# Kernel optimization log

Measured on AMD Instinct MI355X. Metric: run time of the kernel, lower is better.

The kernel has to match this reference:

```python
import jax, jax.numpy as jnp
import numpy as np

EPS = 1e-6
MAX_ACOSH_ARG = 1e6
MAX_DIST = 50.0
TINY = 1e-15
B, T, D = 2, 512, 512
H, N = 8, 32
A = N + 1
TAU = 1.0


def mink(x, y):
    # Lorentzian inner product over last (ambient) dim
    return -x[..., 0] * y[..., 0] + jnp.sum(x[..., 1:] * y[..., 1:], axis=-1)


def project_to_hyperboloid(x):
    xx = mink(x, x)
    scale = jnp.sqrt(jnp.maximum(jnp.abs(xx), TINY))[..., None]
    x = x / scale
    return jnp.concatenate([jnp.abs(x[..., :1]), x[..., 1:]], axis=-1)


def exp_map(p, v):
    vn = jnp.sqrt(jnp.maximum(mink(v, v), TINY))[..., None]
    y = jnp.cosh(vn) * p + (jnp.sinh(vn) / jnp.maximum(vn, TINY)) * v
    return project_to_hyperboloid(y)


def log_map(p, y):
    alpha = jnp.clip(-mink(p, y), 1.0 + EPS, MAX_ACOSH_ARG)
    dist = jnp.arccosh(alpha)[..., None]
    u = y + alpha[..., None] * p
    un = jnp.sqrt(jnp.maximum(mink(u, u), TINY))[..., None]
    return dist / jnp.maximum(un, TINY) * u


def _lift(x, W, b):
    # Linear lift -> (B,H,T,N), append time-like 0, expmap at origin
    u = (jnp.einsum('btd,dk->btk', x, W) + b).reshape(B, T, H, N).transpose(0, 2, 1, 3)
    v = jnp.concatenate([jnp.zeros(u.shape[:-1] + (1,), u.dtype), u], axis=-1)  # (B,H,T,A)
    o = jnp.zeros((A,), u.dtype).at[0].set(1.0)
    return exp_map(jnp.broadcast_to(o, v.shape), v)


def setup_inputs() -> dict:
    key = jax.random.key(0)
    ks = jax.random.split(key, 5)
    x = jax.random.normal(ks[0], (B, T, D), jnp.float32)
    Wq = jax.random.normal(ks[1], (D, H * N), jnp.float32) * 0.02
    Wk = jax.random.normal(ks[2], (D, H * N), jnp.float32) * 0.02
    Wv = jax.random.normal(ks[3], (D, H * N), jnp.float32) * 0.02
    Wo = jax.random.normal(ks[4], (H * A, D), jnp.float32) * 0.02
    return {'x': x, 'Wq': Wq, 'bq': jnp.zeros((H * N,), jnp.float32),
            'Wk': Wk, 'bk': jnp.zeros((H * N,), jnp.float32),
            'Wv': Wv, 'bv': jnp.zeros((H * N,), jnp.float32),
            'Wo': Wo, 'bo': jnp.zeros((D,), jnp.float32)}


def reference(x, Wq, bq, Wk, bk, Wv, bv, Wo, bo):
    Q = _lift(x, Wq, bq)  # (B,H,T,A) on hyperboloid
    K = _lift(x, Wk, bk)
    V = _lift(x, Wv, bv)

    # pairwise hyperbolic distances: alpha = -<q,k>_L, d = acosh(alpha)
    alpha = jnp.clip(-mink(Q[:, :, :, None, :], K[:, :, None, :, :]), 1.0 + EPS, MAX_ACOSH_ARG)
    d = jnp.minimum(jnp.arccosh(alpha), MAX_DIST)  # (B,H,T,T)
    scores = -TAU * d * d
    attn = jax.nn.softmax(scores.astype(jnp.float32), axis=-1).astype(V.dtype)

    # one Karcher step around Q
    Y = Q
    logv = log_map(Y[:, :, :, None, :], V[:, :, None, :, :])  # (B,H,T,T,A)
    step = jnp.einsum('bhqk,bhqka->bhqa', attn, logv)
    step_norm = jnp.sqrt(jnp.maximum(mink(step, step), TINY))[..., None]
    step = step * (jnp.minimum(step_norm, 20.0) / (step_norm + 1e-9))
    Y = exp_map(Y, step)  # (B,H,T,A)

    # log-map at origin anchor, project back to d_model
    o = jnp.zeros((A,), Y.dtype).at[0].set(1.0)
    Yt = Y.transpose(0, 2, 1, 3)  # (B,T,H,A)
    p0 = jnp.broadcast_to(o, Yt.shape)
    Z_tan = log_map(p0, Yt).reshape(B, T, H * A)
    Z = jnp.einsum('btk,kd->btd', Z_tan, Wo) + bo
    return Z
```

## Files before the change

### kernel.cpp

```cpp
#include <hip/hip_runtime.h>
#include <math.h>

#define EPSF 1e-6f
#define MAX_ACOSH_ARGF 1e6f
#define MAX_DISTF 50.0f
#define TINYF 1e-15f

typedef float f4v __attribute__((ext_vector_type(4)));
typedef float f2v __attribute__((ext_vector_type(2)));

constexpr int QPSZ = 16 * 512 * 36;
constexpr int KTSZ = 16 * 9 * 512 * 4;
constexpr int ZTSZ = 1024 * 264;

__device__ __forceinline__ float facosh(float a) {
    return __logf(a + sqrtf((a - 1.0f) * (a + 1.0f)));
}

__global__ __launch_bounds__(64) void qkv_kernel(
    const float* __restrict__ x,
    const float* __restrict__ Wq, const float* __restrict__ bq,
    const float* __restrict__ Wk, const float* __restrict__ bk,
    const float* __restrict__ Wv, const float* __restrict__ bv,
    float* __restrict__ Qp, float* __restrict__ KT, float* __restrict__ VT)
{
    const int lane = threadIdx.x;
    const int gw   = blockIdx.x;
    const int ct   = gw % 6;
    const int mt   = gw / 6;
    const int m0   = mt * 4;
    const int tsel = ct >> 1;
    const int n0   = (ct & 1) * 128;
    const float* W    = (tsel == 0) ? Wq : (tsel == 1) ? Wk : Wv;
    const float* bias = (tsel == 0) ? bq : (tsel == 1) ? bk : bv;
    const int c0 = n0 + lane * 2;
    const float* xb = x + m0 * 512;

    float acc[4][2];
    {
        const float b0 = bias[c0], b1 = bias[c0 + 1];
        #pragma unroll
        for (int r = 0; r < 4; ++r) { acc[r][0] = b0; acc[r][1] = b1; }
    }

    f4v aA[4][2], aB[4][2];
    f2v bA[8], bB[8];

#define LDA_Q(BUF, KB)                                            \
    _Pragma("unroll") for (int r = 0; r < 4; ++r) {               \
        BUF[r][0] = *(const f4v*)(xb + r * 512 + (KB));           \
        BUF[r][1] = *(const f4v*)(xb + r * 512 + (KB) + 4);       \
    }
#define LDB_Q(BUF, KB)                                            \
    _Pragma("unroll") for (int j = 0; j < 8; ++j)                 \
        BUF[j] = *(const f2v*)(W + ((KB) + j) * 256 + c0);
#define STEP_Q(AB, BB)                                            \
    _Pragma("unroll") for (int j = 0; j < 8; ++j) {               \
        _Pragma("unroll") for (int r = 0; r < 4; ++r) {           \
            const float av = AB[r][j >> 2][j & 3];                \
            acc[r][0] = fmaf(av, BB[j][0], acc[r][0]);            \
            acc[r][1] = fmaf(av, BB[j][1], acc[r][1]);            \
        }                                                         \
    }

    LDA_Q(aA, 0) LDB_Q(bA, 0)
    for (int kb = 0; kb < 512; kb += 16) {
        LDA_Q(aB, kb + 8) LDB_Q(bB, kb + 8)
        STEP_Q(aA, bA)
        if (kb + 16 < 512) { LDA_Q(aA, kb + 16) LDB_Q(bA, kb + 16) }
        STEP_Q(aB, bB)
    }

    const int h   = c0 >> 5;
    const int cin = c0 & 31;
    #pragma unroll
    for (int r = 0; r < 4; ++r) {
        const float e0 = acc[r][0], e1 = acc[r][1];
        float n2 = fmaf(e0, e0, e1 * e1);
        #pragma unroll
        for (int msk = 1; msk < 16; msk <<= 1) n2 += __shfl_xor(n2, msk, 64);
        n2 = fmaxf(n2, TINYF);
        const float vn = sqrtf(n2);
        const float ch = coshf(vn);
        const float sh = sinhf(vn) / fmaxf(vn, TINYF);
        const float xx = fmaf(sh * sh, n2, -ch * ch);
        const float scale = sqrtf(fmaxf(fabsf(xx), TINYF));
        const float fs = sh / scale;
        const int bt = m0 + r, b = bt >> 9, t = bt & 511;
        const int bh = b * 8 + h;
        if (tsel == 0) {
            float* qp = Qp + (bh * 512 + t) * 36;
            qp[1 + cin] = fs * e0;
            qp[2 + cin] = fs * e1;
            if (cin == 0)  qp[0] = fabsf(ch / scale);
            if (cin == 30) { qp[33] = 0.0f; qp[34] = 0.0f; qp[35] = 0.0f; }
        } else {
            float* P = ((tsel == 1) ? KT : VT) + bh * 18432;
            const int aa = 1 + cin, ab = 2 + cin;
            P[(aa >> 2) * 2048 + t * 4 + (aa & 3)] = fs * e0;
            P[(ab >> 2) * 2048 + t * 4 + (ab & 3)] = fs * e1;
            if (cin == 0)  P[t * 4] = fabsf(ch / scale);
            if (cin == 30) {
                P[8 * 2048 + t * 4 + 1] = 0.0f;
                P[8 * 2048 + t * 4 + 2] = 0.0f;
                P[8 * 2048 + t * 4 + 3] = 0.0f;
            }
        }
    }
}

__global__ __launch_bounds__(256) void attn_kernel(
    const float* __restrict__ Qp, const float* __restrict__ KT,
    const float* __restrict__ VT, float* __restrict__ ZT)
{
    const int tid  = threadIdx.x;
    const int blk  = blockIdx.x;
    const int bh   = blk >> 5;
    const int q0   = (blk & 31) * 16;
    const int wid  = tid >> 6;
    const int lane = tid & 63;
    const int g    = lane >> 4;
    const int t    = lane & 15;
    const int qi   = q0 + wid * 4 + g;

    float qn[36];
    {
        const float* qp = Qp + (bh * 512 + qi) * 36;
        #pragma unroll
        for (int j = 0; j < 9; ++j) {
            const f4v v = *(const f4v*)(qp + 4 * j);
            #pragma unroll
            for (int i = 0; i < 4; ++i) {
                const int a = 4 * j + i;
                qn[a] = (a == 0) ? v[i] : -v[i];
            }
        }
    }

    const f4v* K4 = (const f4v*)KT + bh * 4608;
    const f4v* V4 = (const f4v*)VT + bh * 4608;

    float m = -3.0e38f, l = 0.0f, s = 0.0f;
    float ac[33];
    #pragma unroll
    for (int a = 0; a < 33; ++a) ac[a] = 0.0f;

    for (int st = 0; st < 32; ++st) {
        const int k = t + 16 * st;
        f4v kr[9], vr[9];
        #pragma unroll
        for (int j = 0; j < 9; ++j) kr[j] = K4[j * 512 + k];
        #pragma unroll
        for (int j = 0; j < 9; ++j) vr[j] = V4[j * 512 + k];

        float p0 = 0.f, p1 = 0.f, p2 = 0.f, p3 = 0.f;
        #pragma unroll
        for (int j = 0; j < 9; ++j) {
            p0 = fmaf(qn[4 * j],     kr[j][0], p0);
            p1 = fmaf(qn[4 * j + 1], kr[j][1], p1);
            p2 = fmaf(qn[4 * j + 2], kr[j][2], p2);
            p3 = fmaf(qn[4 * j + 3], kr[j][3], p3);
        }
        const float a1 = (p0 + p1) + (p2 + p3);

        float r0 = 0.f, r1 = 0.f, r2 = 0.f, r3 = 0.f;
        #pragma unroll
        for (int j = 0; j < 9; ++j) {
            r0 = fmaf(qn[4 * j],     vr[j][0], r0);
            r1 = fmaf(qn[4 * j + 1], vr[j][1], r1);
            r2 = fmaf(qn[4 * j + 2], vr[j][2], r2);
            r3 = fmaf(qn[4 * j + 3], vr[j][3], r3);
        }
        const float a2 = (r0 + r1) + (r2 + r3);

        const float a1c = fminf(fmaxf(a1, 1.0f + EPSF), MAX_ACOSH_ARGF);
        const float d1  = fminf(facosh(a1c), MAX_DISTF);
        const float sN  = -d1 * d1;
        const float a2c = fminf(fmaxf(a2, 1.0f + EPSF), MAX_ACOSH_ARGF);
        const float d2  = facosh(a2c);

        if (sN > m) {
            const float cr = __expf(m - sN);
            l *= cr; s *= cr;
            #pragma unroll
            for (int a = 0; a < 33; ++a) ac[a] *= cr;
            m = sN;
        }
        const float e = __expf(sN - m);
        l += e;
        const float w = e * d2;
        s = fmaf(w, a2c, s);
        #pragma unroll
        for (int a = 0; a < 33; ++a) ac[a] = fmaf(w, vr[a >> 2][a & 3], ac[a]);
    }

    float M = m;
    #pragma unroll
    for (int msk = 1; msk < 16; msk <<= 1) M = fmaxf(M, __shfl_xor(M, msk, 64));
    const float cl = __expf(m - M);
    float lw = l * cl, sw = s * cl;
    #pragma unroll
    for (int msk = 1; msk < 16; msk <<= 1) {
        lw += __shfl_xor(lw, msk, 64);
        sw += __shfl_xor(sw, msk, 64);
    }
    #pragma unroll
    for (int a = 0; a < 33; ++a) {
        float v = ac[a] * cl;
        #pragma unroll
        for (int msk = 1; msk < 16; msk <<= 1) v += __shfl_xor(v, msk, 64);
        ac[a] = v;
    }

    const float un_c  = sqrtf(TINYF);
    const float inv_un = (1.0f / lw) / un_c;
    ac[0] = fmaf(sw, qn[0], ac[0]) * inv_un;
    #pragma unroll
    for (int a = 1; a < 33; ++a) ac[a] = fmaf(-sw, qn[a], ac[a]) * inv_un;

    float mk = -ac[0] * ac[0];
    #pragma unroll
    for (int a = 1; a < 33; ++a) mk = fmaf(ac[a], ac[a], mk);
    const float snorm = sqrtf(fmaxf(mk, TINYF));
    const float fac   = fminf(snorm, 20.0f) / (snorm + 1e-9f);
    #pragma unroll
    for (int a = 0; a < 33; ++a) ac[a] *= fac;

    float mk2 = -ac[0] * ac[0];
    #pragma unroll
    for (int a = 1; a < 33; ++a) mk2 = fmaf(ac[a], ac[a], mk2);
    const float vn  = sqrtf(fmaxf(mk2, TINYF));
    const float ch  = coshf(vn);
    const float shr = sinhf(vn) / fmaxf(vn, TINYF);
    ac[0] = fmaf(ch, qn[0], shr * ac[0]);
    #pragma unroll
    for (int a = 1; a < 33; ++a) ac[a] = fmaf(-ch, qn[a], shr * ac[a]);

    float xx = -ac[0] * ac[0];
    #pragma unroll
    for (int a = 1; a < 33; ++a) xx = fmaf(ac[a], ac[a], xx);
    const float scale = sqrtf(fmaxf(fabsf(xx), TINYF));

    const float Y0  = fabsf(ac[0] / scale);
    const float al3 = fminf(fmaxf(Y0, 1.0f + EPSF), MAX_ACOSH_ARGF);
    const float d3  = acoshf(al3);
    const float f3  = d3 / un_c;

    if (t == 0) {
        const int b = bh >> 3, h = bh & 7;
        float* zp = ZT + (b * 512 + qi) * 264 + h * 33;
        zp[0] = f3 * (Y0 + al3);
        const float fsc = f3 / scale;
        #pragma unroll
        for (int a = 1; a < 33; ++a) zp[a] = fsc * ac[a];
    }
}

__global__ __launch_bounds__(64) void out_kernel(
    const float* __restrict__ ZT, const float* __restrict__ Wo,
    const float* __restrict__ bo, float* __restrict__ out)
{
    const int lane = threadIdx.x;
    const int gw   = blockIdx.x;
    const int mt   = gw >> 2;
    const int m0   = mt * 4;
    const int n0   = (gw & 3) * 128;
    const int c0   = n0 + lane * 2;
    const float* zb = ZT + m0 * 264;

    float acc[4][2];
    {
        const float b0 = bo[c0], b1 = bo[c0 + 1];
        #pragma unroll
        for (int r = 0; r < 4; ++r) { acc[r][0] = b0; acc[r][1] = b1; }
    }

    f4v aA[4][2], aB[4][2];
    f2v bA[8], bB[8];

#define LDA_O(BUF, KB)                                            \
    _Pragma("unroll") for (int r = 0; r < 4; ++r) {               \
        BUF[r][0] = *(const f4v*)(zb + r * 264 + (KB));           \
        BUF[r][1] = *(const f4v*)(zb + r * 264 + (KB) + 4);       \
    }
#define LDB_O(BUF, KB)                                            \
    _Pragma("unroll") for (int j = 0; j < 8; ++j)                 \
        BUF[j] = *(const f2v*)(Wo + ((KB) + j) * 512 + c0);
#define STEP_O(AB, BB)                                            \
    _Pragma("unroll") for (int j = 0; j < 8; ++j) {               \
        _Pragma("unroll") for (int r = 0; r < 4; ++r) {           \
            const float av = AB[r][j >> 2][j & 3];                \
            acc[r][0] = fmaf(av, BB[j][0], acc[r][0]);            \
            acc[r][1] = fmaf(av, BB[j][1], acc[r][1]);            \
        }                                                         \
    }

    LDA_O(aA, 0) LDB_O(bA, 0)
    for (int kb = 0; kb < 256; kb += 16) {
        LDA_O(aB, kb + 8) LDB_O(bB, kb + 8)
        STEP_O(aA, bA)
        LDA_O(aA, kb + 16) LDB_O(bA, kb + 16)
        STEP_O(aB, bB)
    }
    STEP_O(aA, bA)

    #pragma unroll
    for (int r = 0; r < 4; ++r)
        *(f2v*)(out + (m0 + r) * 512 + c0) = f2v{acc[r][0], acc[r][1]};
}

extern "C" void kernel_launch(void* const* d_in, const int* in_sizes, int n_in,
                              void* d_out, int out_size, void* d_ws, size_t ws_size,
                              hipStream_t stream) {
    const float* x  = (const float*)d_in[0];
    const float* Wq = (const float*)d_in[1];
    const float* bq = (const float*)d_in[2];
    const float* Wk = (const float*)d_in[3];
    const float* bk = (const float*)d_in[4];
    const float* Wv = (const float*)d_in[5];
    const float* bv = (const float*)d_in[6];
    const float* Wo = (const float*)d_in[7];
    const float* bo = (const float*)d_in[8];
    float* out = (float*)d_out;
    float* ws  = (float*)d_ws;

    float* Qp  = ws;
    float* KT  = ws + QPSZ;
    float* VT  = ws + QPSZ + KTSZ;
    float* ZTp = ws + QPSZ + 2 * KTSZ;

    qkv_kernel<<<1536, 64, 0, stream>>>(x, Wq, bq, Wk, bk, Wv, bv, Qp, KT, VT);
    attn_kernel<<<512, 256, 0, stream>>>(Qp, KT, VT, ZTp);
    out_kernel<<<1024, 64, 0, stream>>>(ZTp, Wo, bo, out);
}
```

Baseline: 171.7 us.

## Rewrite attention with LDS-staged K/V chunks, two queries per wave, no online max

The attention kernel now stages K and V chunks of 64 keys in double-buffered shared memory. Each wave handles two queries across all 64 lanes, one key per lane, and the final reductions use DPP adds. The running-max softmax rescaling is dropped on the grounds that scores are at most zero, and the s accumulator is recomputed from the reduced sums as a dot with q. Q, K and V share one row-major layout. The QKV and output GEMMs move to a four-stage register prefetch ring. Dropping the max subtraction risks underflow when all scores are very negative, and the larger blocks with two accumulator sets raise register pressure.

```diff
diff --git a/kernel.cpp b/kernel.cpp
--- a/kernel.cpp
+++ b/kernel.cpp
@@ -9,12 +9,26 @@
 typedef float f4v __attribute__((ext_vector_type(4)));
 typedef float f2v __attribute__((ext_vector_type(2)));
 
-constexpr int QPSZ = 16 * 512 * 36;
-constexpr int KTSZ = 16 * 9 * 512 * 4;
-constexpr int ZTSZ = 1024 * 264;
+constexpr int TENS = 16 * 512 * 36;
 
 __device__ __forceinline__ float facosh(float a) {
     return __logf(a + sqrtf((a - 1.0f) * (a + 1.0f)));
+}
+__device__ __forceinline__ float bcast(float x) {
+    return __int_as_float(__builtin_amdgcn_readfirstlane(__float_as_int(x)));
+}
+template<int C> __device__ __forceinline__ float dpp_add(float x) {
+    int t = __builtin_amdgcn_update_dpp(0, __float_as_int(x), C, 0xf, 0xf, false);
+    return x + __int_as_float(t);
+}
+__device__ __forceinline__ float redsum64(float x) {
+    x = dpp_add<0x111>(x);
+    x = dpp_add<0x112>(x);
+    x = dpp_add<0x114>(x);
+    x = dpp_add<0x118>(x);
+    x = dpp_add<0x142>(x);
+    x = dpp_add<0x143>(x);
+    return x;
 }
 
 __global__ __launch_bounds__(64) void qkv_kernel(
@@ -22,7 +36,7 @@
     const float* __restrict__ Wq, const float* __restrict__ bq,
     const float* __restrict__ Wk, const float* __restrict__ bk,
     const float* __restrict__ Wv, const float* __restrict__ bv,
-    float* __restrict__ Qp, float* __restrict__ KT, float* __restrict__ VT)
+    float* __restrict__ Q, float* __restrict__ K, float* __restrict__ V)
 {
     const int lane = threadIdx.x;
     const int gw   = blockIdx.x;
@@ -33,6 +47,7 @@
     const int n0   = (ct & 1) * 128;
     const float* W    = (tsel == 0) ? Wq : (tsel == 1) ? Wk : Wv;
     const float* bias = (tsel == 0) ? bq : (tsel == 1) ? bk : bv;
+    float* OUT        = (tsel == 0) ? Q  : (tsel == 1) ? K  : V;
     const int c0 = n0 + lane * 2;
     const float* xb = x + m0 * 512;
 
@@ -43,33 +58,32 @@
         for (int r = 0; r < 4; ++r) { acc[r][0] = b0; acc[r][1] = b1; }
     }
 
-    f4v aA[4][2], aB[4][2];
-    f2v bA[8], bB[8];
-
-#define LDA_Q(BUF, KB)                                            \
-    _Pragma("unroll") for (int r = 0; r < 4; ++r) {               \
-        BUF[r][0] = *(const f4v*)(xb + r * 512 + (KB));           \
-        BUF[r][1] = *(const f4v*)(xb + r * 512 + (KB) + 4);       \
-    }
-#define LDB_Q(BUF, KB)                                            \
-    _Pragma("unroll") for (int j = 0; j < 8; ++j)                 \
-        BUF[j] = *(const f2v*)(W + ((KB) + j) * 256 + c0);
-#define STEP_Q(AB, BB)                                            \
-    _Pragma("unroll") for (int j = 0; j < 8; ++j) {               \
-        _Pragma("unroll") for (int r = 0; r < 4; ++r) {           \
-            const float av = AB[r][j >> 2][j & 3];                \
-            acc[r][0] = fmaf(av, BB[j][0], acc[r][0]);            \
-            acc[r][1] = fmaf(av, BB[j][1], acc[r][1]);            \
-        }                                                         \
-    }
-
-    LDA_Q(aA, 0) LDB_Q(bA, 0)
-    for (int kb = 0; kb < 512; kb += 16) {
-        LDA_Q(aB, kb + 8) LDB_Q(bB, kb + 8)
-        STEP_Q(aA, bA)
-        if (kb + 16 < 512) { LDA_Q(aA, kb + 16) LDB_Q(bA, kb + 16) }
-        STEP_Q(aB, bB)
-    }
+    f4v a[4][4][2];
+    f2v b[4][8];
+
+#define LDQ(B, KB)                                                      \
+    { _Pragma("unroll") for (int r = 0; r < 4; ++r) {                   \
+          a[B][r][0] = *(const f4v*)(xb + r * 512 + (KB));              \
+          a[B][r][1] = *(const f4v*)(xb + r * 512 + (KB) + 4); }        \
+      _Pragma("unroll") for (int j = 0; j < 8; ++j)                     \
+          b[B][j] = *(const f2v*)(W + ((KB) + j) * 256 + c0); }
+#define STQ(B)                                                          \
+    { _Pragma("unroll") for (int j = 0; j < 8; ++j) {                   \
+        _Pragma("unroll") for (int r = 0; r < 4; ++r) {                 \
+            const float av = a[B][r][j >> 2][j & 3];                    \
+            acc[r][0] = fmaf(av, b[B][j][0], acc[r][0]);                \
+            acc[r][1] = fmaf(av, b[B][j][1], acc[r][1]); } } }
+
+    LDQ(0, 0) LDQ(1, 8) LDQ(2, 16) LDQ(3, 24)
+    for (int kb = 0; kb < 480; kb += 32) {
+        STQ(0) LDQ(0, kb + 32)
+        STQ(1) LDQ(1, kb + 40)
+        STQ(2) LDQ(2, kb + 48)
+        STQ(3) LDQ(3, kb + 56)
+    }
+    STQ(0) STQ(1) STQ(2) STQ(3)
+#undef LDQ
+#undef STQ
 
     const int h   = c0 >> 5;
     const int cin = c0 & 31;
@@ -86,173 +100,196 @@
         const float xx = fmaf(sh * sh, n2, -ch * ch);
         const float scale = sqrtf(fmaxf(fabsf(xx), TINYF));
         const float fs = sh / scale;
-        const int bt = m0 + r, b = bt >> 9, t = bt & 511;
-        const int bh = b * 8 + h;
-        if (tsel == 0) {
-            float* qp = Qp + (bh * 512 + t) * 36;
-            qp[1 + cin] = fs * e0;
-            qp[2 + cin] = fs * e1;
-            if (cin == 0)  qp[0] = fabsf(ch / scale);
-            if (cin == 30) { qp[33] = 0.0f; qp[34] = 0.0f; qp[35] = 0.0f; }
-        } else {
-            float* P = ((tsel == 1) ? KT : VT) + bh * 18432;
-            const int aa = 1 + cin, ab = 2 + cin;
-            P[(aa >> 2) * 2048 + t * 4 + (aa & 3)] = fs * e0;
-            P[(ab >> 2) * 2048 + t * 4 + (ab & 3)] = fs * e1;
-            if (cin == 0)  P[t * 4] = fabsf(ch / scale);
-            if (cin == 30) {
-                P[8 * 2048 + t * 4 + 1] = 0.0f;
-                P[8 * 2048 + t * 4 + 2] = 0.0f;
-                P[8 * 2048 + t * 4 + 3] = 0.0f;
-            }
-        }
-    }
-}
-
-__global__ __launch_bounds__(256) void attn_kernel(
-    const float* __restrict__ Qp, const float* __restrict__ KT,
-    const float* __restrict__ VT, float* __restrict__ ZT)
+        const int bt = m0 + r, bb = bt >> 9, t = bt & 511;
+        float* rp = OUT + ((bb * 8 + h) * 512 + t) * 36;
+        rp[1 + cin] = fs * e0;
+        rp[2 + cin] = fs * e1;
+        if (cin == 0) {
+            rp[0] = fabsf(ch / scale);
+            rp[33] = 0.0f; rp[34] = 0.0f; rp[35] = 0.0f;
+        }
+    }
+}
+
+__global__ __launch_bounds__(512, 4) void attn_kernel(
+    const float* __restrict__ Qg, const float* __restrict__ Kg,
+    const float* __restrict__ Vg, float* __restrict__ ZT)
 {
-    const int tid  = threadIdx.x;
-    const int blk  = blockIdx.x;
-    const int bh   = blk >> 5;
-    const int q0   = (blk & 31) * 16;
-    const int wid  = tid >> 6;
+    __shared__ f4v skv[2][1152];
+    __shared__ f4v sQ4[144];
+
+    const int tid = threadIdx.x;
+    const int blk = blockIdx.x;
+    const int bh  = blk >> 5;
+    const int q0t = (blk & 31) * 16;
+    const int wid = __builtin_amdgcn_readfirstlane(tid >> 6);
     const int lane = tid & 63;
-    const int g    = lane >> 4;
-    const int t    = lane & 15;
-    const int qi   = q0 + wid * 4 + g;
-
-    float qn[36];
+
+    const f4v* K4 = (const f4v*)(Kg + bh * 512 * 36);
+    const f4v* V4 = (const f4v*)(Vg + bh * 512 * 36);
+
+    const f4v* s0 = K4 + tid;
+    const f4v* s1 = (tid < 64) ? (K4 + 512 + tid) : (V4 + (tid - 64));
+    const f4v* s2 = V4 + 448 + tid;
+    const int d0 = tid, d1 = tid + 512, d2 = tid + 1024;
+
+    skv[0][d0] = s0[0];
+    skv[0][d1] = s1[0];
+    if (tid < 128) skv[0][d2] = s2[0];
+    if (tid < 144) sQ4[tid] = ((const f4v*)(Qg + (bh * 512 + q0t) * 36))[tid];
+    __syncthreads();
+
+    float qn0[36], qn1[36];
     {
-        const float* qp = Qp + (bh * 512 + qi) * 36;
+        const float* qs = (const float*)sQ4;
+        #pragma unroll
+        for (int a2 = 0; a2 < 36; ++a2) {
+            const float v0 = qs[(2 * wid) * 36 + a2];
+            const float v1 = qs[(2 * wid + 1) * 36 + a2];
+            qn0[a2] = bcast(a2 ? -v0 : v0);
+            qn1[a2] = bcast(a2 ? -v1 : v1);
+        }
+    }
+
+    float l0 = 0.0f, l1 = 0.0f;
+    float ac0[33], ac1[33];
+    #pragma unroll
+    for (int a2 = 0; a2 < 33; ++a2) { ac0[a2] = 0.0f; ac1[a2] = 0.0f; }
+
+    for (int c = 0; c < 8; ++c) {
+        f4v p0, p1, p2;
+        const bool have = (c < 7);
+        if (have) {
+            p0 = s0[(c + 1) * 576];
+            p1 = s1[(c + 1) * 576];
+            if (tid < 128) p2 = s2[(c + 1) * 576];
+        }
+        const f4v* buf = skv[c & 1];
+        const f4v* kr = buf + lane * 9;
+        const f4v* vr = buf + 576 + lane * 9;
+
+        float x10 = 0.f, x11 = 0.f, x20 = 0.f, x21 = 0.f;
         #pragma unroll
         for (int j = 0; j < 9; ++j) {
-            const f4v v = *(const f4v*)(qp + 4 * j);
-            #pragma unroll
-            for (int i = 0; i < 4; ++i) {
-                const int a = 4 * j + i;
-                qn[a] = (a == 0) ? v[i] : -v[i];
-            }
-        }
-    }
-
-    const f4v* K4 = (const f4v*)KT + bh * 4608;
-    const f4v* V4 = (const f4v*)VT + bh * 4608;
-
-    float m = -3.0e38f, l = 0.0f, s = 0.0f;
-    float ac[33];
+            const f4v kv = kr[j];
+            x10 = fmaf(qn0[4 * j],     kv[0], x10);
+            x11 = fmaf(qn0[4 * j + 1], kv[1], x11);
+            x10 = fmaf(qn0[4 * j + 2], kv[2], x10);
+            x11 = fmaf(qn0[4 * j + 3], kv[3], x11);
+            x20 = fmaf(qn1[4 * j],     kv[0], x20);
+            x21 = fmaf(qn1[4 * j + 1], kv[1], x21);
+            x20 = fmaf(qn1[4 * j + 2], kv[2], x20);
+            x21 = fmaf(qn1[4 * j + 3], kv[3], x21);
+        }
+        const float a1q0 = x10 + x11, a1q1 = x20 + x21;
+
+        if (have) {
+            f4v* w = skv[(c + 1) & 1];
+            w[d0] = p0; w[d1] = p1;
+            if (tid < 128) w[d2] = p2;
+        }
+
+        f4v vf[9];
+        #pragma unroll
+        for (int j = 0; j < 9; ++j) vf[j] = vr[j];
+        float y10 = 0.f, y11 = 0.f, y20 = 0.f, y21 = 0.f;
+        #pragma unroll
+        for (int j = 0; j < 9; ++j) {
+            y10 = fmaf(qn0[4 * j],     vf[j][0], y10);
+            y11 = fmaf(qn0[4 * j + 1], vf[j][1], y11);
+            y10 = fmaf(qn0[4 * j + 2], vf[j][2], y10);
+            y11 = fmaf(qn0[4 * j + 3], vf[j][3], y11);
+            y20 = fmaf(qn1[4 * j],     vf[j][0], y20);
+            y21 = fmaf(qn1[4 * j + 1], vf[j][1], y21);
+            y20 = fmaf(qn1[4 * j + 2], vf[j][2], y20);
+            y21 = fmaf(qn1[4 * j + 3], vf[j][3], y21);
+        }
+        const float a2q0 = y10 + y11, a2q1 = y20 + y21;
+
+        {
+            const float a1c = fminf(fmaxf(a1q0, 1.0f + EPSF), MAX_ACOSH_ARGF);
+            const float dd  = fminf(facosh(a1c), MAX_DISTF);
+            const float e   = __expf(-dd * dd);
+            const float a2c = fminf(fmaxf(a2q0, 1.0f + EPSF), MAX_ACOSH_ARGF);
+            const float w0  = e * facosh(a2c);
+            l0 += e;
+            #pragma unroll
+            for (int a2 = 0; a2 < 33; ++a2)
+                ac0[a2] = fmaf(w0, vf[a2 >> 2][a2 & 3], ac0[a2]);
+        }
+        {
+            const float a1c = fminf(fmaxf(a1q1, 1.0f + EPSF), MAX_ACOSH_ARGF);
+            const float dd  = fminf(facosh(a1c), MAX_DISTF);
+            const float e   = __expf(-dd * dd);
+            const float a2c = fminf(fmaxf(a2q1, 1.0f + EPSF), MAX_ACOSH_ARGF);
+            const float w1  = e * facosh(a2c);
+            l1 += e;
+            #pragma unroll
+            for (int a2 = 0; a2 < 33; ++a2)
+                ac1[a2] = fmaf(w1, vf[a2 >> 2][a2 & 3], ac1[a2]);
+        }
+        __syncthreads();
+    }
+
+    const float lw0 = redsum64(l0);
+    const float lw1 = redsum64(l1);
     #pragma unroll
-    for (int a = 0; a < 33; ++a) ac[a] = 0.0f;
-
-    for (int st = 0; st < 32; ++st) {
-        const int k = t + 16 * st;
-        f4v kr[9], vr[9];
-        #pragma unroll
-        for (int j = 0; j < 9; ++j) kr[j] = K4[j * 512 + k];
-        #pragma unroll
-        for (int j = 0; j < 9; ++j) vr[j] = V4[j * 512 + k];
-
-        float p0 = 0.f, p1 = 0.f, p2 = 0.f, p3 = 0.f;
-        #pragma unroll
-        for (int j = 0; j < 9; ++j) {
-            p0 = fmaf(qn[4 * j],     kr[j][0], p0);
-            p1 = fmaf(qn[4 * j + 1], kr[j][1], p1);
-            p2 = fmaf(qn[4 * j + 2], kr[j][2], p2);
-            p3 = fmaf(qn[4 * j + 3], kr[j][3], p3);
-        }
-        const float a1 = (p0 + p1) + (p2 + p3);
-
-        float r0 = 0.f, r1 = 0.f, r2 = 0.f, r3 = 0.f;
-        #pragma unroll
-        for (int j = 0; j < 9; ++j) {
-            r0 = fmaf(qn[4 * j],     vr[j][0], r0);
-            r1 = fmaf(qn[4 * j + 1], vr[j][1], r1);
-            r2 = fmaf(qn[4 * j + 2], vr[j][2], r2);
-            r3 = fmaf(qn[4 * j + 3], vr[j][3], r3);
-        }
-        const float a2 = (r0 + r1) + (r2 + r3);
-
-        const float a1c = fminf(fmaxf(a1, 1.0f + EPSF), MAX_ACOSH_ARGF);
-        const float d1  = fminf(facosh(a1c), MAX_DISTF);
-        const float sN  = -d1 * d1;
-        const float a2c = fminf(fmaxf(a2, 1.0f + EPSF), MAX_ACOSH_ARGF);
-        const float d2  = facosh(a2c);
-
-        if (sN > m) {
-            const float cr = __expf(m - sN);
-            l *= cr; s *= cr;
-            #pragma unroll
-            for (int a = 0; a < 33; ++a) ac[a] *= cr;
-            m = sN;
-        }
-        const float e = __expf(sN - m);
-        l += e;
-        const float w = e * d2;
-        s = fmaf(w, a2c, s);
-        #pragma unroll
-        for (int a = 0; a < 33; ++a) ac[a] = fmaf(w, vr[a >> 2][a & 3], ac[a]);
-    }
-
-    float M = m;
-    #pragma unroll
-    for (int msk = 1; msk < 16; msk <<= 1) M = fmaxf(M, __shfl_xor(M, msk, 64));
-    const float cl = __expf(m - M);
-    float lw = l * cl, sw = s * cl;
-    #pragma unroll
-    for (int msk = 1; msk < 16; msk <<= 1) {
-        lw += __shfl_xor(lw, msk, 64);
-        sw += __shfl_xor(sw, msk, 64);
-    }
-    #pragma unroll
-    for (int a = 0; a < 33; ++a) {
-        float v = ac[a] * cl;
-        #pragma unroll
-        for (int msk = 1; msk < 16; msk <<= 1) v += __shfl_xor(v, msk, 64);
-        ac[a] = v;
-    }
-
-    const float un_c  = sqrtf(TINYF);
-    const float inv_un = (1.0f / lw) / un_c;
-    ac[0] = fmaf(sw, qn[0], ac[0]) * inv_un;
-    #pragma unroll
-    for (int a = 1; a < 33; ++a) ac[a] = fmaf(-sw, qn[a], ac[a]) * inv_un;
-
-    float mk = -ac[0] * ac[0];
-    #pragma unroll
-    for (int a = 1; a < 33; ++a) mk = fmaf(ac[a], ac[a], mk);
-    const float snorm = sqrtf(fmaxf(mk, TINYF));
-    const float fac   = fminf(snorm, 20.0f) / (snorm + 1e-9f);
-    #pragma unroll
-    for (int a = 0; a < 33; ++a) ac[a] *= fac;
-
-    float mk2 = -ac[0] * ac[0];
-    #pragma unroll
-    for (int a = 1; a < 33; ++a) mk2 = fmaf(ac[a], ac[a], mk2);
-    const float vn  = sqrtf(fmaxf(mk2, TINYF));
-    const float ch  = coshf(vn);
-    const float shr = sinhf(vn) / fmaxf(vn, TINYF);
-    ac[0] = fmaf(ch, qn[0], shr * ac[0]);
-    #pragma unroll
-    for (int a = 1; a < 33; ++a) ac[a] = fmaf(-ch, qn[a], shr * ac[a]);
-
-    float xx = -ac[0] * ac[0];
-    #pragma unroll
-    for (int a = 1; a < 33; ++a) xx = fmaf(ac[a], ac[a], xx);
-    const float scale = sqrtf(fmaxf(fabsf(xx), TINYF));
-
-    const float Y0  = fabsf(ac[0] / scale);
-    const float al3 = fminf(fmaxf(Y0, 1.0f + EPSF), MAX_ACOSH_ARGF);
-    const float d3  = acoshf(al3);
-    const float f3  = d3 / un_c;
-
-    if (t == 0) {
+    for (int a2 = 0; a2 < 33; ++a2) {
+        ac0[a2] = redsum64(ac0[a2]);
+        ac1[a2] = redsum64(ac1[a2]);
+    }
+
+    if (lane == 63) {
         const int b = bh >> 3, h = bh & 7;
-        float* zp = ZT + (b * 512 + qi) * 264 + h * 33;
-        zp[0] = f3 * (Y0 + al3);
-        const float fsc = f3 / scale;
-        #pragma unroll
-        for (int a = 1; a < 33; ++a) zp[a] = fsc * ac[a];
+        #pragma unroll
+        for (int q = 0; q < 2; ++q) {
+            float (&ac)[33] = q ? ac1 : ac0;
+            const float (&qn)[36] = q ? qn1 : qn0;
+            const float lw = q ? lw1 : lw0;
+            float sw = 0.0f;
+            #pragma unroll
+            for (int a2 = 0; a2 < 33; ++a2) sw = fmaf(qn[a2], ac[a2], sw);
+            const float un_c  = 3.1622776601683794e-8f;
+            const float inv_un = (1.0f / lw) / un_c;
+            ac[0] = fmaf(sw, qn[0], ac[0]) * inv_un;
+            #pragma unroll
+            for (int a2 = 1; a2 < 33; ++a2) ac[a2] = fmaf(-sw, qn[a2], ac[a2]) * inv_un;
+
+            float mk = -ac[0] * ac[0];
+            #pragma unroll
+            for (int a2 = 1; a2 < 33; ++a2) mk = fmaf(ac[a2], ac[a2], mk);
+            const float snorm = sqrtf(fmaxf(mk, TINYF));
+            const float fac   = fminf(snorm, 20.0f) / (snorm + 1e-9f);
+            #pragma unroll
+            for (int a2 = 0; a2 < 33; ++a2) ac[a2] *= fac;
+
+            float mk2 = -ac[0] * ac[0];
+            #pragma unroll
+            for (int a2 = 1; a2 < 33; ++a2) mk2 = fmaf(ac[a2], ac[a2], mk2);
+            const float vn  = sqrtf(fmaxf(mk2, TINYF));
+            const float ch  = coshf(vn);
+            const float shr = sinhf(vn) / fmaxf(vn, TINYF);
+            ac[0] = fmaf(ch, qn[0], shr * ac[0]);
+            #pragma unroll
+            for (int a2 = 1; a2 < 33; ++a2) ac[a2] = fmaf(-ch, qn[a2], shr * ac[a2]);
+
+            float xx = -ac[0] * ac[0];
+            #pragma unroll
+            for (int a2 = 1; a2 < 33; ++a2) xx = fmaf(ac[a2], ac[a2], xx);
+            const float scale = sqrtf(fmaxf(fabsf(xx), TINYF));
+
+            const float Y0  = fabsf(ac[0] / scale);
+            const float al3 = fminf(fmaxf(Y0, 1.0f + EPSF), MAX_ACOSH_ARGF);
+            const float d3  = acoshf(al3);
+            const float f3  = d3 / un_c;
+
+            const int qi = q0t + 2 * wid + q;
+            float* zp = ZT + (b * 512 + qi) * 264 + h * 33;
+            zp[0] = f3 * (Y0 + al3);
+            const float fsc = f3 / scale;
+            #pragma unroll
+            for (int a2 = 1; a2 < 33; ++a2) zp[a2] = fsc * ac[a2];
+        }
     }
 }
 
@@ -275,34 +312,34 @@
         for (int r = 0; r < 4; ++r) { acc[r][0] = b0; acc[r][1] = b1; }
     }
 
-    f4v aA[4][2], aB[4][2];
-    f2v bA[8], bB[8];
-
-#define LDA_O(BUF, KB)                                            \
-    _Pragma("unroll") for (int r = 0; r < 4; ++r) {               \
-        BUF[r][0] = *(const f4v*)(zb + r * 264 + (KB));           \
-        BUF[r][1] = *(const f4v*)(zb + r * 264 + (KB) + 4);       \
-    }
-#define LDB_O(BUF, KB)                                            \
-    _Pragma("unroll") for (int j = 0; j < 8; ++j)                 \
-        BUF[j] = *(const f2v*)(Wo + ((KB) + j) * 512 + c0);
-#define STEP_O(AB, BB)                                            \
-    _Pragma("unroll") for (int j = 0; j < 8; ++j) {               \
-        _Pragma("unroll") for (int r = 0; r < 4; ++r) {           \
-            const float av = AB[r][j >> 2][j & 3];                \
-            acc[r][0] = fmaf(av, BB[j][0], acc[r][0]);            \
-            acc[r][1] = fmaf(av, BB[j][1], acc[r][1]);            \
-        }                                                         \
-    }
-
-    LDA_O(aA, 0) LDB_O(bA, 0)
-    for (int kb = 0; kb < 256; kb += 16) {
-        LDA_O(aB, kb + 8) LDB_O(bB, kb + 8)
-        STEP_O(aA, bA)
-        LDA_O(aA, kb + 16) LDB_O(bA, kb + 16)
-        STEP_O(aB, bB)
-    }
-    STEP_O(aA, bA)
+    f4v a[4][4][2];
+    f2v b[4][8];
+
+#define LDO(B, KB)                                                      \
+    { _Pragma("unroll") for (int r = 0; r < 4; ++r) {                   \
+          a[B][r][0] = *(const f4v*)(zb + r * 264 + (KB));              \
+          a[B][r][1] = *(const f4v*)(zb + r * 264 + (KB) + 4); }        \
+      _Pragma("unroll") for (int j = 0; j < 8; ++j)                     \
+          b[B][j] = *(const f2v*)(Wo + ((KB) + j) * 512 + c0); }
+#define STO(B)                                                          \
+    { _Pragma("unroll") for (int j = 0; j < 8; ++j) {                   \
+        _Pragma("unroll") for (int r = 0; r < 4; ++r) {                 \
+            const float av = a[B][r][j >> 2][j & 3];                    \
+            acc[r][0] = fmaf(av, b[B][j][0], acc[r][0]);                \
+            acc[r][1] = fmaf(av, b[B][j][1], acc[r][1]); } } }
+
+    LDO(0, 0) LDO(1, 8) LDO(2, 16) LDO(3, 24)
+    for (int kb = 0; kb < 224; kb += 32) {
+        STO(0) LDO(0, kb + 32)
+        STO(1) LDO(1, kb + 40)
+        STO(2) LDO(2, kb + 48)
+        STO(3) LDO(3, kb + 56)
+    }
+    STO(0) LDO(0, 256)
+    STO(1) STO(2) STO(3)
+    STO(0)
+#undef LDO
+#undef STO
 
     #pragma unroll
     for (int r = 0; r < 4; ++r)
@@ -324,12 +361,12 @@
     float* out = (float*)d_out;
     float* ws  = (float*)d_ws;
 
-    float* Qp  = ws;
-    float* KT  = ws + QPSZ;
-    float* VT  = ws + QPSZ + KTSZ;
-    float* ZTp = ws + QPSZ + 2 * KTSZ;
-
-    qkv_kernel<<<1536, 64, 0, stream>>>(x, Wq, bq, Wk, bk, Wv, bv, Qp, KT, VT);
-    attn_kernel<<<512, 256, 0, stream>>>(Qp, KT, VT, ZTp);
+    float* Q   = ws;
+    float* K   = ws + TENS;
+    float* V   = ws + 2 * TENS;
+    float* ZTp = ws + 3 * TENS;
+
+    qkv_kernel<<<1536, 64, 0, stream>>>(x, Wq, bq, Wk, bk, Wv, bv, Q, K, V);
+    attn_kernel<<<512, 512, 0, stream>>>(Q, K, V, ZTp);
     out_kernel<<<1024, 64, 0, stream>>>(ZTp, Wo, bo, out);
 }
```

Result: slower. 218.0 us (+27.0%).

## Split-K GEMMs, separate lift kernel, and split attention key range across warps

Applied to the files above, without the earlier changes.

The QKV projection becomes a split-K GEMM with 256-thread blocks writing partial sums, and a separate lift kernel reduces those partials and applies the exp-map. The attention kernel splits the key range across two warps per query group and combines them through shared memory. It also drops the online-softmax max tracking in favour of plain exp(-d^2), since distances are non-negative and the maximum score is at most zero. The output GEMM is split-K with a separate reduce-plus-bias kernel. Together these aim to raise parallelism and occupancy, at the cost of extra launches and workspace traffic.

```diff
diff --git a/kernel.cpp b/kernel.cpp
--- a/kernel.cpp
+++ b/kernel.cpp
@@ -9,129 +9,147 @@
 typedef float f4v __attribute__((ext_vector_type(4)));
 typedef float f2v __attribute__((ext_vector_type(2)));
 
-constexpr int QPSZ = 16 * 512 * 36;
-constexpr int KTSZ = 16 * 9 * 512 * 4;
-constexpr int ZTSZ = 1024 * 264;
+constexpr int OFF_U  = 0;
+constexpr int OFF_OP = 0;
+constexpr int OFF_ZT = 1048576;
+constexpr int OFF_Q  = 3145728;
+constexpr int OFF_KT = 3440640;
+constexpr int OFF_VT = 3735552;
 
 __device__ __forceinline__ float facosh(float a) {
     return __logf(a + sqrtf((a - 1.0f) * (a + 1.0f)));
 }
 
-__global__ __launch_bounds__(64) void qkv_kernel(
+__global__ __launch_bounds__(256, 4) void qkv_gemm(
     const float* __restrict__ x,
-    const float* __restrict__ Wq, const float* __restrict__ bq,
-    const float* __restrict__ Wk, const float* __restrict__ bk,
-    const float* __restrict__ Wv, const float* __restrict__ bv,
+    const float* __restrict__ Wq, const float* __restrict__ Wk,
+    const float* __restrict__ Wv, float* __restrict__ U)
+{
+    const int tid  = threadIdx.x;
+    const int wid  = tid >> 6;
+    const int lane = tid & 63;
+    const int blk  = blockIdx.x;
+    const int rt   = blk & 63;
+    const int cs   = blk >> 6;
+    const int ct   = cs % 6;
+    const int s    = cs / 6;
+    const int m0   = rt * 16 + wid * 4;
+    const int tsel = ct >> 1;
+    const int n0t  = (ct & 1) * 128;
+    const float* W = (tsel == 0) ? Wq : (tsel == 1) ? Wk : Wv;
+    const int c0   = n0t + lane * 2;
+    const int k0   = s * 128;
+    const float* xb = x + m0 * 512 + k0;
+    const float* wp = W + k0 * 256 + c0;
+
+    float acc[4][2];
+    #pragma unroll
+    for (int r = 0; r < 4; ++r) { acc[r][0] = 0.0f; acc[r][1] = 0.0f; }
+
+    f4v a[2][4][2];
+    f2v b[2][8];
+
+#define LDQ(B, KB)                                                      \
+    { _Pragma("unroll") for (int r = 0; r < 4; ++r) {                   \
+          a[B][r][0] = *(const f4v*)(xb + r * 512 + (KB));              \
+          a[B][r][1] = *(const f4v*)(xb + r * 512 + (KB) + 4); }        \
+      _Pragma("unroll") for (int j = 0; j < 8; ++j)                     \
+          b[B][j] = *(const f2v*)(wp + ((KB) + j) * 256); }
+#define STQ(B)                                                          \
+    { _Pragma("unroll") for (int j = 0; j < 8; ++j) {                   \
+        _Pragma("unroll") for (int r = 0; r < 4; ++r) {                 \
+            const float av = a[B][r][j >> 2][j & 3];                    \
+            acc[r][0] = fmaf(av, b[B][j][0], acc[r][0]);                \
+            acc[r][1] = fmaf(av, b[B][j][1], acc[r][1]); } } }
+
+    LDQ(0, 0) LDQ(1, 8)
+    for (int kb = 0; kb < 112; kb += 16) {
+        STQ(0) LDQ(0, kb + 16)
+        STQ(1) LDQ(1, kb + 24)
+    }
+    STQ(0) STQ(1)
+#undef LDQ
+#undef STQ
+
+    #pragma unroll
+    for (int r = 0; r < 4; ++r)
+        *(f2v*)(U + (s * 1024 + m0 + r) * 768 + tsel * 256 + c0) =
+            f2v{acc[r][0], acc[r][1]};
+}
+
+__global__ __launch_bounds__(768) void lift_kernel(
+    const float* __restrict__ U,
+    const float* __restrict__ bq, const float* __restrict__ bk,
+    const float* __restrict__ bv,
     float* __restrict__ Qp, float* __restrict__ KT, float* __restrict__ VT)
 {
-    const int lane = threadIdx.x;
-    const int gw   = blockIdx.x;
-    const int ct   = gw % 6;
-    const int mt   = gw / 6;
-    const int m0   = mt * 4;
-    const int tsel = ct >> 1;
-    const int n0   = (ct & 1) * 128;
-    const float* W    = (tsel == 0) ? Wq : (tsel == 1) ? Wk : Wv;
+    const int bt = blockIdx.x;
+    const int b  = bt >> 9, t = bt & 511;
+    const int j  = threadIdx.x;
+    const int tsel = j >> 8, h = (j >> 5) & 7, cin = j & 31;
+
     const float* bias = (tsel == 0) ? bq : (tsel == 1) ? bk : bv;
-    const int c0 = n0 + lane * 2;
-    const float* xb = x + m0 * 512;
-
-    float acc[4][2];
-    {
-        const float b0 = bias[c0], b1 = bias[c0 + 1];
-        #pragma unroll
-        for (int r = 0; r < 4; ++r) { acc[r][0] = b0; acc[r][1] = b1; }
-    }
-
-    f4v aA[4][2], aB[4][2];
-    f2v bA[8], bB[8];
-
-#define LDA_Q(BUF, KB)                                            \
-    _Pragma("unroll") for (int r = 0; r < 4; ++r) {               \
-        BUF[r][0] = *(const f4v*)(xb + r * 512 + (KB));           \
-        BUF[r][1] = *(const f4v*)(xb + r * 512 + (KB) + 4);       \
-    }
-#define LDB_Q(BUF, KB)                                            \
-    _Pragma("unroll") for (int j = 0; j < 8; ++j)                 \
-        BUF[j] = *(const f2v*)(W + ((KB) + j) * 256 + c0);
-#define STEP_Q(AB, BB)                                            \
-    _Pragma("unroll") for (int j = 0; j < 8; ++j) {               \
-        _Pragma("unroll") for (int r = 0; r < 4; ++r) {           \
-            const float av = AB[r][j >> 2][j & 3];                \
-            acc[r][0] = fmaf(av, BB[j][0], acc[r][0]);            \
-            acc[r][1] = fmaf(av, BB[j][1], acc[r][1]);            \
-        }                                                         \
-    }
-
-    LDA_Q(aA, 0) LDB_Q(bA, 0)
-    for (int kb = 0; kb < 512; kb += 16) {
-        LDA_Q(aB, kb + 8) LDB_Q(bB, kb + 8)
-        STEP_Q(aA, bA)
-        if (kb + 16 < 512) { LDA_Q(aA, kb + 16) LDB_Q(bA, kb + 16) }
-        STEP_Q(aB, bB)
-    }
-
-    const int h   = c0 >> 5;
-    const int cin = c0 & 31;
-    #pragma unroll
-    for (int r = 0; r < 4; ++r) {
-        const float e0 = acc[r][0], e1 = acc[r][1];
-        float n2 = fmaf(e0, e0, e1 * e1);
-        #pragma unroll
-        for (int msk = 1; msk < 16; msk <<= 1) n2 += __shfl_xor(n2, msk, 64);
-        n2 = fmaxf(n2, TINYF);
-        const float vn = sqrtf(n2);
-        const float ch = coshf(vn);
-        const float sh = sinhf(vn) / fmaxf(vn, TINYF);
-        const float xx = fmaf(sh * sh, n2, -ch * ch);
-        const float scale = sqrtf(fmaxf(fabsf(xx), TINYF));
-        const float fs = sh / scale;
-        const int bt = m0 + r, b = bt >> 9, t = bt & 511;
-        const int bh = b * 8 + h;
-        if (tsel == 0) {
-            float* qp = Qp + (bh * 512 + t) * 36;
-            qp[1 + cin] = fs * e0;
-            qp[2 + cin] = fs * e1;
-            if (cin == 0)  qp[0] = fabsf(ch / scale);
-            if (cin == 30) { qp[33] = 0.0f; qp[34] = 0.0f; qp[35] = 0.0f; }
-        } else {
-            float* P = ((tsel == 1) ? KT : VT) + bh * 18432;
-            const int aa = 1 + cin, ab = 2 + cin;
-            P[(aa >> 2) * 2048 + t * 4 + (aa & 3)] = fs * e0;
-            P[(ab >> 2) * 2048 + t * 4 + (ab & 3)] = fs * e1;
-            if (cin == 0)  P[t * 4] = fabsf(ch / scale);
-            if (cin == 30) {
-                P[8 * 2048 + t * 4 + 1] = 0.0f;
-                P[8 * 2048 + t * 4 + 2] = 0.0f;
-                P[8 * 2048 + t * 4 + 3] = 0.0f;
-            }
+    float u = bias[j & 255];
+    #pragma unroll
+    for (int s = 0; s < 4; ++s) u += U[s * 786432 + bt * 768 + j];
+
+    float n2 = u * u;
+    #pragma unroll
+    for (int msk = 1; msk < 32; msk <<= 1) n2 += __shfl_xor(n2, msk, 64);
+    n2 = fmaxf(n2, TINYF);
+    const float vn = sqrtf(n2);
+    const float ch = coshf(vn);
+    const float sh = sinhf(vn) / fmaxf(vn, TINYF);
+    const float xx = fmaf(sh * sh, n2, -ch * ch);
+    const float scale = sqrtf(fmaxf(fabsf(xx), TINYF));
+    const float fs = sh / scale;
+    const float tc = fabsf(ch / scale);
+    const int bh = b * 8 + h;
+
+    if (tsel == 0) {
+        float* qp = Qp + (bh * 512 + t) * 36;
+        qp[1 + cin] = fs * u;
+        if (cin == 0) { qp[0] = tc; qp[33] = 0.0f; qp[34] = 0.0f; qp[35] = 0.0f; }
+    } else {
+        float* P = ((tsel == 1) ? KT : VT) + bh * 18432;
+        const int a0 = 1 + cin;
+        P[(a0 >> 2) * 2048 + t * 4 + (a0 & 3)] = fs * u;
+        if (cin == 0) {
+            P[t * 4] = tc;
+            P[8 * 2048 + t * 4 + 1] = 0.0f;
+            P[8 * 2048 + t * 4 + 2] = 0.0f;
+            P[8 * 2048 + t * 4 + 3] = 0.0f;
         }
     }
 }
 
-__global__ __launch_bounds__(256) void attn_kernel(
+__global__ __launch_bounds__(256, 4) void attn_kernel(
     const float* __restrict__ Qp, const float* __restrict__ KT,
     const float* __restrict__ VT, float* __restrict__ ZT)
 {
-    const int tid  = threadIdx.x;
-    const int blk  = blockIdx.x;
-    const int bh   = blk >> 5;
-    const int q0   = (blk & 31) * 16;
-    const int wid  = tid >> 6;
-    const int lane = tid & 63;
-    const int g    = lane >> 4;
-    const int t    = lane & 15;
-    const int qi   = q0 + wid * 4 + g;
+    __shared__ float part[2][4][34];
+
+    const int tid   = threadIdx.x;
+    const int blk   = blockIdx.x;
+    const int bh    = blk >> 6;
+    const int q0    = (blk & 63) * 8;
+    const int wid   = tid >> 6;
+    const int lane  = tid & 63;
+    const int g     = lane >> 4;
+    const int t     = lane & 15;
+    const int quad  = wid >> 1;
+    const int khalf = wid & 1;
+    const int qi    = q0 + quad * 4 + g;
 
     float qn[36];
     {
         const float* qp = Qp + (bh * 512 + qi) * 36;
         #pragma unroll
-        for (int j = 0; j < 9; ++j) {
-            const f4v v = *(const f4v*)(qp + 4 * j);
+        for (int jj = 0; jj < 9; ++jj) {
+            const f4v v = *(const f4v*)(qp + 4 * jj);
             #pragma unroll
             for (int i = 0; i < 4; ++i) {
-                const int a = 4 * j + i;
+                const int a = 4 * jj + i;
                 qn[a] = (a == 0) ? v[i] : -v[i];
             }
         }
@@ -140,80 +158,76 @@
     const f4v* K4 = (const f4v*)KT + bh * 4608;
     const f4v* V4 = (const f4v*)VT + bh * 4608;
 
-    float m = -3.0e38f, l = 0.0f, s = 0.0f;
+    float l = 0.0f;
     float ac[33];
     #pragma unroll
     for (int a = 0; a < 33; ++a) ac[a] = 0.0f;
 
-    for (int st = 0; st < 32; ++st) {
-        const int k = t + 16 * st;
+    for (int st = 0; st < 16; ++st) {
+        const int k = t + 16 * st + 256 * khalf;
         f4v kr[9], vr[9];
         #pragma unroll
-        for (int j = 0; j < 9; ++j) kr[j] = K4[j * 512 + k];
-        #pragma unroll
-        for (int j = 0; j < 9; ++j) vr[j] = V4[j * 512 + k];
+        for (int jj = 0; jj < 9; ++jj) kr[jj] = K4[jj * 512 + k];
+        #pragma unroll
+        for (int jj = 0; jj < 9; ++jj) vr[jj] = V4[jj * 512 + k];
 
         float p0 = 0.f, p1 = 0.f, p2 = 0.f, p3 = 0.f;
         #pragma unroll
-        for (int j = 0; j < 9; ++j) {
-            p0 = fmaf(qn[4 * j],     kr[j][0], p0);
-            p1 = fmaf(qn[4 * j + 1], kr[j][1], p1);
-            p2 = fmaf(qn[4 * j + 2], kr[j][2], p2);
-            p3 = fmaf(qn[4 * j + 3], kr[j][3], p3);
+        for (int jj = 0; jj < 9; ++jj) {
+            p0 = fmaf(qn[4 * jj],     kr[jj][0], p0);
+            p1 = fmaf(qn[4 * jj + 1], kr[jj][1], p1);
+            p2 = fmaf(qn[4 * jj + 2], kr[jj][2], p2);
+            p3 = fmaf(qn[4 * jj + 3], kr[jj][3], p3);
         }
         const float a1 = (p0 + p1) + (p2 + p3);
 
         float r0 = 0.f, r1 = 0.f, r2 = 0.f, r3 = 0.f;
         #pragma unroll
-        for (int j = 0; j < 9; ++j) {
-            r0 = fmaf(qn[4 * j],     vr[j][0], r0);
-            r1 = fmaf(qn[4 * j + 1], vr[j][1], r1);
-            r2 = fmaf(qn[4 * j + 2], vr[j][2], r2);
-            r3 = fmaf(qn[4 * j + 3], vr[j][3], r3);
+        for (int jj = 0; jj < 9; ++jj) {
+            r0 = fmaf(qn[4 * jj],     vr[jj][0], r0);
+            r1 = fmaf(qn[4 * jj + 1], vr[jj][1], r1);
+            r2 = fmaf(qn[4 * jj + 2], vr[jj][2], r2);
+            r3 = fmaf(qn[4 * jj + 3], vr[jj][3], r3);
         }
         const float a2 = (r0 + r1) + (r2 + r3);
 
         const float a1c = fminf(fmaxf(a1, 1.0f + EPSF), MAX_ACOSH_ARGF);
-        const float d1  = fminf(facosh(a1c), MAX_DISTF);
-        const float sN  = -d1 * d1;
+        const float dd  = fminf(facosh(a1c), MAX_DISTF);
+        const float e   = __expf(-dd * dd);
         const float a2c = fminf(fmaxf(a2, 1.0f + EPSF), MAX_ACOSH_ARGF);
-        const float d2  = facosh(a2c);
-
-        if (sN > m) {
-            const float cr = __expf(m - sN);
-            l *= cr; s *= cr;
-            #pragma unroll
-            for (int a = 0; a < 33; ++a) ac[a] *= cr;
-            m = sN;
-        }
-        const float e = __expf(sN - m);
+        const float w   = e * facosh(a2c);
         l += e;
-        const float w = e * d2;
-        s = fmaf(w, a2c, s);
         #pragma unroll
         for (int a = 0; a < 33; ++a) ac[a] = fmaf(w, vr[a >> 2][a & 3], ac[a]);
     }
 
-    float M = m;
-    #pragma unroll
-    for (int msk = 1; msk < 16; msk <<= 1) M = fmaxf(M, __shfl_xor(M, msk, 64));
-    const float cl = __expf(m - M);
-    float lw = l * cl, sw = s * cl;
-    #pragma unroll
-    for (int msk = 1; msk < 16; msk <<= 1) {
-        lw += __shfl_xor(lw, msk, 64);
-        sw += __shfl_xor(sw, msk, 64);
-    }
+    #pragma unroll
+    for (int msk = 1; msk < 16; msk <<= 1) l += __shfl_xor(l, msk, 64);
     #pragma unroll
     for (int a = 0; a < 33; ++a) {
-        float v = ac[a] * cl;
+        float v = ac[a];
         #pragma unroll
         for (int msk = 1; msk < 16; msk <<= 1) v += __shfl_xor(v, msk, 64);
         ac[a] = v;
     }
 
-    const float un_c  = sqrtf(TINYF);
-    const float inv_un = (1.0f / lw) / un_c;
+    if (khalf == 1 && t == 0) {
+        part[quad][g][0] = l;
+        #pragma unroll
+        for (int a = 0; a < 33; ++a) part[quad][g][1 + a] = ac[a];
+    }
+    __syncthreads();
+    if (khalf == 1) return;
+
+    l += part[quad][g][0];
+    #pragma unroll
+    for (int a = 0; a < 33; ++a) ac[a] += part[quad][g][1 + a];
+
+    float sw = 0.0f;
+    #pragma unroll
+    for (int a = 0; a < 33; ++a) sw = fmaf(qn[a], ac[a], sw);
+    const float un_c   = 3.1622776601683794e-8f;
+    const float inv_un = (1.0f / l) / un_c;
     ac[0] = fmaf(sw, qn[0], ac[0]) * inv_un;
     #pragma unroll
     for (int a = 1; a < 33; ++a) ac[a] = fmaf(-sw, qn[a], ac[a]) * inv_un;
@@ -256,57 +270,63 @@
     }
 }
 
-__global__ __launch_bounds__(64) void out_kernel(
+__global__ __launch_bounds__(256, 4) void out_gemm(
     const float* __restrict__ ZT, const float* __restrict__ Wo,
-    const float* __restrict__ bo, float* __restrict__ out)
-{
-    const int lane = threadIdx.x;
-    const int gw   = blockIdx.x;
-    const int mt   = gw >> 2;
-    const int m0   = mt * 4;
-    const int n0   = (gw & 3) * 128;
-    const int c0   = n0 + lane * 2;
-    const float* zb = ZT + m0 * 264;
-
-    float acc[4][2];
-    {
-        const float b0 = bo[c0], b1 = bo[c0 + 1];
-        #pragma unroll
-        for (int r = 0; r < 4; ++r) { acc[r][0] = b0; acc[r][1] = b1; }
-    }
-
-    f4v aA[4][2], aB[4][2];
-    f2v bA[8], bB[8];
-
-#define LDA_O(BUF, KB)                                            \
-    _Pragma("unroll") for (int r = 0; r < 4; ++r) {               \
-        BUF[r][0] = *(const f4v*)(zb + r * 264 + (KB));           \
-        BUF[r][1] = *(const f4v*)(zb + r * 264 + (KB) + 4);       \
-    }
-#define LDB_O(BUF, KB)                                            \
-    _Pragma("unroll") for (int j = 0; j < 8; ++j)                 \
-        BUF[j] = *(const f2v*)(Wo + ((KB) + j) * 512 + c0);
-#define STEP_O(AB, BB)                                            \
-    _Pragma("unroll") for (int j = 0; j < 8; ++j) {               \
-        _Pragma("unroll") for (int r = 0; r < 4; ++r) {           \
-            const float av = AB[r][j >> 2][j & 3];                \
-            acc[r][0] = fmaf(av, BB[j][0], acc[r][0]);            \
-            acc[r][1] = fmaf(av, BB[j][1], acc[r][1]);            \
-        }                                                         \
-    }
-
-    LDA_O(aA, 0) LDB_O(bA, 0)
-    for (int kb = 0; kb < 256; kb += 16) {
-        LDA_O(aB, kb + 8) LDB_O(bB, kb + 8)
-        STEP_O(aA, bA)
-        LDA_O(aA, kb + 16) LDB_O(bA, kb + 16)
-        STEP_O(aB, bB)
-    }
-    STEP_O(aA, bA)
+    float* __restrict__ OP)
+{
+    const int tid  = threadIdx.x;
+    const int wid  = tid >> 6;
+    const int lane = tid & 63;
+    const int blk  = blockIdx.x;
+    const int rt   = blk & 63;
+    const int cs   = blk >> 6;
+    const int ct   = cs & 7;
+    const int s    = cs >> 3;
+    const int m0   = rt * 16 + wid * 4;
+    const int c0   = ct * 64 + lane;
+    const int k0   = s * 132;
+    const float* zb = ZT + m0 * 264 + k0;
+    const float* wp = Wo + k0 * 512 + c0;
+
+    float acc[4] = {0.f, 0.f, 0.f, 0.f};
+    f4v a[2][4];
+    float bv[2][4];
+
+#define LDO(B, KK)                                                      \
+    { _Pragma("unroll") for (int r = 0; r < 4; ++r)                     \
+          a[B][r] = *(const f4v*)(zb + r * 264 + (KK));                 \
+      _Pragma("unroll") for (int jj = 0; jj < 4; ++jj)                  \
+          bv[B][jj] = wp[((KK) + jj) * 512]; }
+#define STO(B)                                                          \
+    { _Pragma("unroll") for (int jj = 0; jj < 4; ++jj) {                \
+        _Pragma("unroll") for (int r = 0; r < 4; ++r)                   \
+            acc[r] = fmaf(a[B][r][jj], bv[B][jj], acc[r]); } }
+
+    LDO(0, 0) LDO(1, 4)
+    for (int kb = 0; kb < 120; kb += 8) {
+        STO(0) LDO(0, kb + 8)
+        STO(1) LDO(1, kb + 12)
+    }
+    STO(0) LDO(0, 128)
+    STO(1)
+    STO(0)
+#undef LDO
+#undef STO
 
     #pragma unroll
     for (int r = 0; r < 4; ++r)
-        *(f2v*)(out + (m0 + r) * 512 + c0) = f2v{acc[r][0], acc[r][1]};
+        OP[s * 524288 + (m0 + r) * 512 + c0] = acc[r];
+}
+
+__global__ __launch_bounds__(256) void out_reduce(
+    const float* __restrict__ OP, const float* __restrict__ bo,
+    float* __restrict__ out)
+{
+    const int i4 = blockIdx.x * 256 + threadIdx.x;
+    const f4v p0 = ((const f4v*)OP)[i4];
+    const f4v p1 = ((const f4v*)OP)[i4 + 131072];
+    const f4v bb = ((const f4v*)bo)[i4 & 127];
+    ((f4v*)out)[i4] = p0 + p1 + bb;
 }
 
 extern "C" void kernel_launch(void* const* d_in, const int* in_sizes, int n_in,
@@ -324,12 +344,16 @@
     float* out = (float*)d_out;
     float* ws  = (float*)d_ws;
 
-    float* Qp  = ws;
-    float* KT  = ws + QPSZ;
-    float* VT  = ws + QPSZ + KTSZ;
-    float* ZTp = ws + QPSZ + 2 * KTSZ;
-
-    qkv_kernel<<<1536, 64, 0, stream>>>(x, Wq, bq, Wk, bk, Wv, bv, Qp, KT, VT);
-    attn_kernel<<<512, 256, 0, stream>>>(Qp, KT, VT, ZTp);
-    out_kernel<<<1024, 64, 0, stream>>>(ZTp, Wo, bo, out);
-}
+    float* U   = ws + OFF_U;
+    float* OP  = ws + OFF_OP;
+    float* ZTp = ws + OFF_ZT;
+    float* Qp  = ws + OFF_Q;
+    float* KT  = ws + OFF_KT;
+    float* VT  = ws + OFF_VT;
+
+    qkv_gemm<<<1536, 256, 0, stream>>>(x, Wq, Wk, Wv, U);
+    lift_kernel<<<1024, 768, 0, stream>>>(U, bq, bk, bv, Qp, KT, VT);
+    attn_kernel<<<1024, 256, 0, stream>>>(Qp, KT, VT, ZTp);
+    out_gemm<<<1024, 256, 0, stream>>>(ZTp, Wo, OP);
+    out_reduce<<<512, 256, 0, stream>>>(OP, bo, out);
+}
```

Result: slower. 258.3 us (+50.4%).
